# Kernel tuning notes

Hardware: AMD Instinct MI355X
Metric: run time of the kernel (lower is better)

## Reference

```python
import jax, jax.numpy as jnp
import numpy as np

WINDOW_SIZES = (128, 256, 512)
EMBED_DIM = 512
B, T = 128, 65536


def _branch_tokens(signal, W, b, w):
    # Conv1d(in=1, out=E, kernel=w, stride=w, padding=0) == non-overlapping
    # patch projection: (B, S, w) @ (w, E) with S = T // w.
    Bsz, Tlen = signal.shape
    S = Tlen // w
    patches = signal[:, : S * w].reshape(Bsz, S, w)
    return jnp.einsum('bsw,ew->bse', patches, W) + b  # (B, S, E)


def setup_inputs() -> dict:
    key = jax.random.key(0)
    ks = jax.random.split(key, 9)
    signal = jax.random.normal(ks[0], (B, T), dtype=jnp.float32)
    signal_mask = jax.random.randint(ks[1], (B, T), 0, 2).astype(bool)
    branch_idx = jax.random.randint(ks[2], (B,), 0, len(WINDOW_SIZES), dtype=jnp.int32)
    params = {}
    for i, w in enumerate(WINDOW_SIZES):
        params[f'W{i}'] = jax.random.normal(ks[3 + 2 * i], (EMBED_DIM, w), dtype=jnp.float32) * 0.02
        params[f'b{i}'] = jax.random.normal(ks[4 + 2 * i], (EMBED_DIM,), dtype=jnp.float32) * 0.02
    return {'signal': signal, 'signal_mask': signal_mask, 'branch_idx': branch_idx, **params}


def reference(signal, signal_mask, branch_idx, W0, b0, W1, b1, W2, b2):
    Bsz, Tlen = signal.shape
    Ws = (W0, W1, W2)
    bs = (b0, b1, b2)
    branch_S = [Tlen // w for w in WINDOW_SIZES]
    S_max = max(branch_S)
    # Compute every branch for every sample (faithful to the original module).
    padded = []
    for w, Wi, bi, Si in zip(WINDOW_SIZES, Ws, bs, branch_S):
        t = _branch_tokens(signal, Wi, bi, w)  # (B, Si, E)
        padded.append(jnp.pad(t, ((0, 0), (0, S_max - Si), (0, 0))))
    stacked = jnp.stack(padded)  # (n_branches, B, S_max, E)
    gathered = stacked[branch_idx, jnp.arange(Bsz)]  # (B, S_max, E)

    lengths = signal_mask.astype(jnp.int32).sum(axis=1)  # (B,)
    w_arr = jnp.asarray(WINDOW_SIZES, dtype=jnp.int32)
    S_arr = jnp.asarray(branch_S, dtype=jnp.int32)
    n_valid = jnp.minimum(lengths // w_arr[branch_idx],
                          jnp.minimum(S_arr[branch_idx], S_max))  # (B,)
    padding_mask = jnp.arange(S_max, dtype=jnp.int32)[None, :] < n_valid[:, None]  # (B, S_max)
    tokens = jnp.where(padding_mask[..., None], gathered, jnp.zeros((), signal.dtype))
    return tokens, padding_mask
```

## Files before the change

### kernel.cpp

```cpp
#include <hip/hip_runtime.h>
#include <hip/hip_bf16.h>

#define BATCH 128
#define TLEN  65536
#define EDIM  512
#define SMAX  512

typedef __attribute__((ext_vector_type(8))) short   bf16x8;
typedef __attribute__((ext_vector_type(4))) float   floatx4;
typedef __attribute__((ext_vector_type(8))) ushort  ushort8;

#define LDS_STRIDE 40
#define BUFSZ (128 * LDS_STRIDE)

__device__ __forceinline__ ushort f2bf(float f) {
  __hip_bfloat16 h = __float2bfloat16(f);
  return *reinterpret_cast<ushort*>(&h);
}

__device__ __forceinline__ void cvt16(ushort* dst, float4 a, float4 b,
                                      float4 c, float4 d) {
  ushort8 p0, p1;
  p0[0]=f2bf(a.x); p0[1]=f2bf(a.y); p0[2]=f2bf(a.z); p0[3]=f2bf(a.w);
  p0[4]=f2bf(b.x); p0[5]=f2bf(b.y); p0[6]=f2bf(b.z); p0[7]=f2bf(b.w);
  p1[0]=f2bf(c.x); p1[1]=f2bf(c.y); p1[2]=f2bf(c.z); p1[3]=f2bf(c.w);
  p1[4]=f2bf(d.x); p1[5]=f2bf(d.y); p1[6]=f2bf(d.z); p1[7]=f2bf(d.w);
  *(ushort8*)dst = p0; *(ushort8*)(dst + 8) = p1;
}

__global__ __launch_bounds__(256) void mask_partial_kernel(
    const int* __restrict__ mask, int* __restrict__ part) {
  const int b = blockIdx.x, c = blockIdx.y, t = threadIdx.x;
  const int4* row = (const int4*)(mask + (size_t)b * TLEN + (size_t)c * 8192);
  int s = 0;
  #pragma unroll
  for (int i = 0; i < 8; ++i) {
    int4 v = row[t + i * 256];
    s += (v.x != 0) + (v.y != 0) + (v.z != 0) + (v.w != 0);
  }
  #pragma unroll
  for (int off = 32; off > 0; off >>= 1) s += __shfl_down(s, off);
  __shared__ int partial[4];
  if ((t & 63) == 0) partial[t >> 6] = s;
  __syncthreads();
  if (t == 0)
    part[b * 8 + c] = partial[0] + partial[1] + partial[2] + partial[3];
}

__global__ __launch_bounds__(256) void mask_final_kernel(
    const int* __restrict__ part, const int* __restrict__ branch_idx,
    int* __restrict__ n_valid, float* __restrict__ out_mask) {
  const int b = blockIdx.x, t = threadIdx.x;
  __shared__ int nv_sh;
  if (t == 0) {
    int len = 0;
    #pragma unroll
    for (int i = 0; i < 8; ++i) len += part[b * 8 + i];
    int w = 128 << branch_idx[b];
    int nv = len / w;
    n_valid[b] = nv;
    nv_sh = nv;
  }
  __syncthreads();
  const int nv = nv_sh;
  out_mask[(size_t)b * SMAX + t]       = (t < nv)       ? 1.0f : 0.0f;
  out_mask[(size_t)b * SMAX + 256 + t] = (256 + t < nv) ? 1.0f : 0.0f;
}

template <int W>
__device__ __forceinline__ void gemm_body(
    const float* __restrict__ sigb, const float* __restrict__ Wp,
    const float* __restrict__ bp, float* __restrict__ outb,
    int nv, int s0, int e0, int t, ushort* Ab, ushort* Bb) {
  constexpr int ITERS = W / 32;
  const int wave   = t >> 6;
  const int lane   = t & 63;
  const int lane16 = lane & 15;
  const int quad   = lane >> 4;
  const int ws_ = (wave >> 1) * 64;
  const int we_ = (wave & 1) * 64;
  const int r = t >> 1, h = t & 1;

  const float* asrc = sigb + (size_t)(s0 + r) * W + h * 16;
  const float* bsrc = Wp + (size_t)(e0 + r) * W + h * 16;
  ushort* adst = Ab + r * LDS_STRIDE + h * 16;
  ushort* bdst = Bb + r * LDS_STRIDE + h * 16;

  float4 av0, av1, av2, av3, bv0, bv1, bv2, bv3;
  {
    const float4* a4 = (const float4*)asrc;
    const float4* b4 = (const float4*)bsrc;
    av0 = a4[0]; av1 = a4[1]; av2 = a4[2]; av3 = a4[3];
    bv0 = b4[0]; bv1 = b4[1]; bv2 = b4[2]; bv3 = b4[3];
  }
  cvt16(adst, av0, av1, av2, av3);
  cvt16(bdst, bv0, bv1, bv2, bv3);
  __syncthreads();

  floatx4 acc[4][4];
  #pragma unroll
  for (int i = 0; i < 4; ++i)
    #pragma unroll
    for (int j = 0; j < 4; ++j) acc[i][j] = (floatx4)(0.f);

  #pragma unroll
  for (int k = 0; k < ITERS; ++k) {
    const ushort* curA = Ab + (k & 1) * BUFSZ;
    const ushort* curB = Bb + (k & 1) * BUFSZ;
    if (k + 1 < ITERS) {
      const float4* a4 = (const float4*)(asrc + (k + 1) * 32);
      const float4* b4 = (const float4*)(bsrc + (k + 1) * 32);
      av0 = a4[0]; av1 = a4[1]; av2 = a4[2]; av3 = a4[3];
      bv0 = b4[0]; bv1 = b4[1]; bv2 = b4[2]; bv3 = b4[3];
    }
    bf16x8 af[4], bfr[4];
    #pragma unroll
    for (int i = 0; i < 4; ++i)
      af[i] = *(const bf16x8*)&curA[(ws_ + i * 16 + lane16) * LDS_STRIDE + quad * 8];
    #pragma unroll
    for (int j = 0; j < 4; ++j)
      bfr[j] = *(const bf16x8*)&curB[(we_ + j * 16 + lane16) * LDS_STRIDE + quad * 8];
    #pragma unroll
    for (int i = 0; i < 4; ++i)
      #pragma unroll
      for (int j = 0; j < 4; ++j)
        acc[i][j] = __builtin_amdgcn_mfma_f32_16x16x32_bf16(af[i], bfr[j], acc[i][j], 0, 0, 0);
    if (k + 1 < ITERS) {
      ushort* nA = Ab + ((k + 1) & 1) * BUFSZ + r * LDS_STRIDE + h * 16;
      ushort* nB = Bb + ((k + 1) & 1) * BUFSZ + r * LDS_STRIDE + h * 16;
      cvt16(nA, av0, av1, av2, av3);
      cvt16(nB, bv0, bv1, bv2, bv3);
      __syncthreads();
    }
  }

  float bval[4];
  #pragma unroll
  for (int j = 0; j < 4; ++j) bval[j] = bp[e0 + we_ + j * 16 + lane16];
  #pragma unroll
  for (int i = 0; i < 4; ++i) {
    #pragma unroll
    for (int rr = 0; rr < 4; ++rr) {
      const int s_row = s0 + ws_ + i * 16 + quad * 4 + rr;
      const bool valid = s_row < nv;
      float* op = outb + (size_t)s_row * EDIM + e0 + we_ + lane16;
      #pragma unroll
      for (int j = 0; j < 4; ++j)
        op[j * 16] = valid ? (acc[i][j][rr] + bval[j]) : 0.f;
    }
  }
}

__global__ __launch_bounds__(256) void gemm_kernel(
    const float* __restrict__ signal, const int* __restrict__ branch_idx,
    const int* __restrict__ n_valid_arr,
    const float* __restrict__ W0, const float* __restrict__ bias0,
    const float* __restrict__ W1, const float* __restrict__ bias1,
    const float* __restrict__ W2, const float* __restrict__ bias2,
    float* __restrict__ out) {
  const int et = blockIdx.x;
  const int st = blockIdx.y;
  const int b  = blockIdx.z;
  const int t  = threadIdx.x;
  const int s0 = st * 128;
  const int e0 = et * 128;
  const int bi = branch_idx[b];
  const int S_b = 512 >> bi;
  float* outb = out + (size_t)b * SMAX * EDIM;

  if (s0 >= S_b) {
    const float4 z = make_float4(0.f, 0.f, 0.f, 0.f);
    #pragma unroll
    for (int i = 0; i < 16; ++i) {
      int idx = t + i * 256;
      int r = idx >> 5, c = idx & 31;
      *(float4*)(outb + (size_t)(s0 + r) * EDIM + e0 + c * 4) = z;
    }
    return;
  }

  __shared__ __align__(16) ushort Ab[2 * BUFSZ];
  __shared__ __align__(16) ushort Bb[2 * BUFSZ];
  const int nv = n_valid_arr[b];
  const float* sigb = signal + (size_t)b * TLEN;

  switch (bi) {
    case 0:
      gemm_body<128>(sigb, W0, bias0, outb, nv, s0, e0, t, Ab, Bb);
      break;
    case 1:
      gemm_body<256>(sigb, W1, bias1, outb, nv, s0, e0, t, Ab, Bb);
      break;
    default:
      gemm_body<512>(sigb, W2, bias2, outb, nv, s0, e0, t, Ab, Bb);
      break;
  }
}

extern "C" void kernel_launch(void* const* d_in, const int* in_sizes, int n_in,
                              void* d_out, int out_size, void* d_ws, size_t ws_size,
                              hipStream_t stream) {
  const float* signal = (const float*)d_in[0];
  const int*   mask   = (const int*)d_in[1];
  const int*   bidx   = (const int*)d_in[2];
  const float* W0 = (const float*)d_in[3];
  const float* b0 = (const float*)d_in[4];
  const float* W1 = (const float*)d_in[5];
  const float* b1 = (const float*)d_in[6];
  const float* W2 = (const float*)d_in[7];
  const float* b2 = (const float*)d_in[8];

  float* out_tokens = (float*)d_out;
  float* out_mask   = (float*)d_out + (size_t)BATCH * SMAX * EDIM;
  int*   n_valid    = (int*)d_ws;
  int*   part       = (int*)d_ws + 128;

  mask_partial_kernel<<<dim3(BATCH, 8), dim3(256), 0, stream>>>(mask, part);
  mask_final_kernel<<<dim3(BATCH), dim3(256), 0, stream>>>(part, bidx, n_valid, out_mask);
  gemm_kernel<<<dim3(4, 4, BATCH), dim3(256), 0, stream>>>(
      signal, bidx, n_valid, W0, b0, W1, b1, W2, b2, out_tokens);
}
```

Measured before the change: 262.3 us.

## Pre-convert inputs to bf16 and stream tiles via global_load_lds with swizzle

Adds a separate pass that converts the whole signal and all weight matrices to bf16 in workspace. The GEMM then loads tiles directly into LDS using global_load_lds with an XOR-swizzled layout, removing per-tile register conversion. This costs an extra full read of the fp32 signal (32 MB) plus a 16 MB write, and the GEMM then reads the bf16 copy back. The old fp32 path remains as a fallback when the workspace is too small.

```diff
diff --git a/kernel.cpp b/kernel.cpp
--- a/kernel.cpp
+++ b/kernel.cpp
@@ -9,9 +9,6 @@
 typedef __attribute__((ext_vector_type(8))) short   bf16x8;
 typedef __attribute__((ext_vector_type(4))) float   floatx4;
 typedef __attribute__((ext_vector_type(8))) ushort  ushort8;
-
-#define LDS_STRIDE 40
-#define BUFSZ (128 * LDS_STRIDE)
 
 __device__ __forceinline__ ushort f2bf(float f) {
   __hip_bfloat16 h = __float2bfloat16(f);
@@ -28,6 +25,12 @@
   *(ushort8*)dst = p0; *(ushort8*)(dst + 8) = p1;
 }
 
+__device__ __forceinline__ void gl_lds16(const ushort* g, ushort* l) {
+  __builtin_amdgcn_global_load_lds(
+      (const __attribute__((address_space(1))) void*)g,
+      (__attribute__((address_space(3))) void*)l, 16, 0, 0);
+}
+
 __global__ __launch_bounds__(256) void mask_partial_kernel(
     const int* __restrict__ mask, int* __restrict__ part) {
   const int b = blockIdx.x, c = blockIdx.y, t = threadIdx.x;
@@ -67,71 +70,84 @@
   out_mask[(size_t)b * SMAX + 256 + t] = (256 + t < nv) ? 1.0f : 0.0f;
 }
 
+#define SIGN  (BATCH * TLEN)
+#define W0N   (EDIM * 128)
+#define W1N   (EDIM * 256)
+#define W2N   (EDIM * 512)
+#define CVT_TOTAL (SIGN + W0N + W1N + W2N)
+
+__global__ __launch_bounds__(256) void cvt_kernel(
+    const float* __restrict__ sig, const float* __restrict__ W0,
+    const float* __restrict__ W1, const float* __restrict__ W2,
+    ushort* __restrict__ dst) {
+  const size_t i = ((size_t)blockIdx.x * 256 + threadIdx.x) * 16;
+  const float* src;
+  if (i < SIGN)                  src = sig + i;
+  else if (i < SIGN + W0N)       src = W0 + (i - SIGN);
+  else if (i < SIGN + W0N + W1N) src = W1 + (i - SIGN - W0N);
+  else                           src = W2 + (i - SIGN - W0N - W1N);
+  const float4* s4 = (const float4*)src;
+  cvt16(dst + i, s4[0], s4[1], s4[2], s4[3]);
+}
+
 template <int W>
-__device__ __forceinline__ void gemm_body(
-    const float* __restrict__ sigb, const float* __restrict__ Wp,
+__device__ __forceinline__ void gemm_mfma_body(
+    const ushort* __restrict__ sigb, const ushort* __restrict__ Wp,
     const float* __restrict__ bp, float* __restrict__ outb,
-    int nv, int s0, int e0, int t, ushort* Ab, ushort* Bb) {
+    int nv, int s0, int e0, int t, ushort* Abuf, ushort* Bbuf) {
   constexpr int ITERS = W / 32;
-  const int wave   = t >> 6;
-  const int lane   = t & 63;
-  const int lane16 = lane & 15;
-  const int quad   = lane >> 4;
-  const int ws_ = (wave >> 1) * 64;
-  const int we_ = (wave & 1) * 64;
-  const int r = t >> 1, h = t & 1;
-
-  const float* asrc = sigb + (size_t)(s0 + r) * W + h * 16;
-  const float* bsrc = Wp + (size_t)(e0 + r) * W + h * 16;
-  ushort* adst = Ab + r * LDS_STRIDE + h * 16;
-  ushort* bdst = Bb + r * LDS_STRIDE + h * 16;
-
-  float4 av0, av1, av2, av3, bv0, bv1, bv2, bv3;
+  const int wave = t >> 6, lane = t & 63;
+  const int lane16 = lane & 15, quad = lane >> 4;
+  const int ws_ = (wave >> 1) * 64, we_ = (wave & 1) * 64;
+
+  const int c0 = t,        r0 = c0 >> 2, kc0 = (c0 & 3) ^ (r0 & 3);
+  const int c1 = t + 256,  r1 = c1 >> 2, kc1 = (c1 & 3) ^ (r1 & 3);
+  const ushort* ag0 = sigb + (size_t)(s0 + r0) * W + kc0 * 8;
+  const ushort* ag1 = sigb + (size_t)(s0 + r1) * W + kc1 * 8;
+  const ushort* bg0 = Wp + (size_t)(e0 + r0) * W + kc0 * 8;
+  const ushort* bg1 = Wp + (size_t)(e0 + r1) * W + kc1 * 8;
+  ushort* al0 = Abuf + wave * 512;
+  ushort* al1 = Abuf + 2048 + wave * 512;
+  ushort* bl0 = Bbuf + wave * 512;
+  ushort* bl1 = Bbuf + 2048 + wave * 512;
+
+  floatx4 acc[4][4];
+  #pragma unroll
+  for (int i = 0; i < 4; ++i)
+    #pragma unroll
+    for (int j = 0; j < 4; ++j) acc[i][j] = (floatx4)(0.f);
+
   {
-    const float4* a4 = (const float4*)asrc;
-    const float4* b4 = (const float4*)bsrc;
-    av0 = a4[0]; av1 = a4[1]; av2 = a4[2]; av3 = a4[3];
-    bv0 = b4[0]; bv1 = b4[1]; bv2 = b4[2]; bv3 = b4[3];
-  }
-  cvt16(adst, av0, av1, av2, av3);
-  cvt16(bdst, bv0, bv1, bv2, bv3);
+    gl_lds16(ag0, al0); gl_lds16(ag1, al1);
+    gl_lds16(bg0, bl0); gl_lds16(bg1, bl1);
+  }
   __syncthreads();
 
-  floatx4 acc[4][4];
-  #pragma unroll
-  for (int i = 0; i < 4; ++i)
-    #pragma unroll
-    for (int j = 0; j < 4; ++j) acc[i][j] = (floatx4)(0.f);
+  const int slotq = (quad ^ (lane16 & 3)) * 8;
 
   #pragma unroll
   for (int k = 0; k < ITERS; ++k) {
-    const ushort* curA = Ab + (k & 1) * BUFSZ;
-    const ushort* curB = Bb + (k & 1) * BUFSZ;
     if (k + 1 < ITERS) {
-      const float4* a4 = (const float4*)(asrc + (k + 1) * 32);
-      const float4* b4 = (const float4*)(bsrc + (k + 1) * 32);
-      av0 = a4[0]; av1 = a4[1]; av2 = a4[2]; av3 = a4[3];
-      bv0 = b4[0]; bv1 = b4[1]; bv2 = b4[2]; bv3 = b4[3];
-    }
+      const size_t ko = (size_t)(k + 1) * 32;
+      const int p = ((k + 1) & 1) * 4096;
+      gl_lds16(ag0 + ko, al0 + p); gl_lds16(ag1 + ko, al1 + p);
+      gl_lds16(bg0 + ko, bl0 + p); gl_lds16(bg1 + ko, bl1 + p);
+    }
+    const ushort* A = Abuf + (k & 1) * 4096;
+    const ushort* B = Bbuf + (k & 1) * 4096;
     bf16x8 af[4], bfr[4];
     #pragma unroll
     for (int i = 0; i < 4; ++i)
-      af[i] = *(const bf16x8*)&curA[(ws_ + i * 16 + lane16) * LDS_STRIDE + quad * 8];
+      af[i] = *(const bf16x8*)&A[(ws_ + i * 16 + lane16) * 32 + slotq];
     #pragma unroll
     for (int j = 0; j < 4; ++j)
-      bfr[j] = *(const bf16x8*)&curB[(we_ + j * 16 + lane16) * LDS_STRIDE + quad * 8];
+      bfr[j] = *(const bf16x8*)&B[(we_ + j * 16 + lane16) * 32 + slotq];
     #pragma unroll
     for (int i = 0; i < 4; ++i)
       #pragma unroll
       for (int j = 0; j < 4; ++j)
         acc[i][j] = __builtin_amdgcn_mfma_f32_16x16x32_bf16(af[i], bfr[j], acc[i][j], 0, 0, 0);
-    if (k + 1 < ITERS) {
-      ushort* nA = Ab + ((k + 1) & 1) * BUFSZ + r * LDS_STRIDE + h * 16;
-      ushort* nB = Bb + ((k + 1) & 1) * BUFSZ + r * LDS_STRIDE + h * 16;
-      cvt16(nA, av0, av1, av2, av3);
-      cvt16(nB, bv0, bv1, bv2, bv3);
-      __syncthreads();
-    }
+    __syncthreads();
   }
 
   float bval[4];
@@ -151,23 +167,128 @@
   }
 }
 
-__global__ __launch_bounds__(256) void gemm_kernel(
+__global__ __launch_bounds__(256) void gemm_bf_kernel(
+    const ushort* __restrict__ sigbf, const int* __restrict__ branch_idx,
+    const int* __restrict__ n_valid_arr,
+    const ushort* __restrict__ W0b, const float* __restrict__ bias0,
+    const ushort* __restrict__ W1b, const float* __restrict__ bias1,
+    const ushort* __restrict__ W2b, const float* __restrict__ bias2,
+    float* __restrict__ out) {
+  const int et = blockIdx.x, st = blockIdx.y, b = blockIdx.z;
+  const int t = threadIdx.x;
+  const int s0 = st * 128, e0 = et * 128;
+  const int bi = branch_idx[b];
+  const int S_b = 512 >> bi;
+  float* outb = out + (size_t)b * SMAX * EDIM;
+
+  if (s0 >= S_b) {
+    const float4 z = make_float4(0.f, 0.f, 0.f, 0.f);
+    #pragma unroll
+    for (int i = 0; i < 16; ++i) {
+      int idx = t + i * 256;
+      int r = idx >> 5, c = idx & 31;
+      *(float4*)(outb + (size_t)(s0 + r) * EDIM + e0 + c * 4) = z;
+    }
+    return;
+  }
+
+  __shared__ __align__(16) ushort Abuf[2 * 4096];
+  __shared__ __align__(16) ushort Bbuf[2 * 4096];
+  const int nv = n_valid_arr[b];
+  const ushort* sigb = sigbf + (size_t)b * TLEN;
+  switch (bi) {
+    case 0:  gemm_mfma_body<128>(sigb, W0b, bias0, outb, nv, s0, e0, t, Abuf, Bbuf); break;
+    case 1:  gemm_mfma_body<256>(sigb, W1b, bias1, outb, nv, s0, e0, t, Abuf, Bbuf); break;
+    default: gemm_mfma_body<512>(sigb, W2b, bias2, outb, nv, s0, e0, t, Abuf, Bbuf); break;
+  }
+}
+
+#define LDS_STRIDE 40
+#define BUFSZ (128 * LDS_STRIDE)
+
+template <int W>
+__device__ __forceinline__ void gemm_fb_body(
+    const float* __restrict__ sigb, const float* __restrict__ Wp,
+    const float* __restrict__ bp, float* __restrict__ outb,
+    int nv, int s0, int e0, int t, ushort* Ab, ushort* Bb) {
+  constexpr int ITERS = W / 32;
+  const int wave = t >> 6, lane = t & 63;
+  const int lane16 = lane & 15, quad = lane >> 4;
+  const int ws_ = (wave >> 1) * 64, we_ = (wave & 1) * 64;
+  const int r = t >> 1, h = t & 1;
+  const float* asrc = sigb + (size_t)(s0 + r) * W + h * 16;
+  const float* bsrc = Wp + (size_t)(e0 + r) * W + h * 16;
+  {
+    const float4* a4 = (const float4*)asrc;
+    const float4* b4 = (const float4*)bsrc;
+    cvt16(Ab + r * LDS_STRIDE + h * 16, a4[0], a4[1], a4[2], a4[3]);
+    cvt16(Bb + r * LDS_STRIDE + h * 16, b4[0], b4[1], b4[2], b4[3]);
+  }
+  __syncthreads();
+  floatx4 acc[4][4];
+  #pragma unroll
+  for (int i = 0; i < 4; ++i)
+    #pragma unroll
+    for (int j = 0; j < 4; ++j) acc[i][j] = (floatx4)(0.f);
+  #pragma unroll
+  for (int k = 0; k < ITERS; ++k) {
+    const ushort* curA = Ab + (k & 1) * BUFSZ;
+    const ushort* curB = Bb + (k & 1) * BUFSZ;
+    float4 av0, av1, av2, av3, bv0, bv1, bv2, bv3;
+    if (k + 1 < ITERS) {
+      const float4* a4 = (const float4*)(asrc + (k + 1) * 32);
+      const float4* b4 = (const float4*)(bsrc + (k + 1) * 32);
+      av0 = a4[0]; av1 = a4[1]; av2 = a4[2]; av3 = a4[3];
+      bv0 = b4[0]; bv1 = b4[1]; bv2 = b4[2]; bv3 = b4[3];
+    }
+    bf16x8 af[4], bfr[4];
+    #pragma unroll
+    for (int i = 0; i < 4; ++i)
+      af[i] = *(const bf16x8*)&curA[(ws_ + i * 16 + lane16) * LDS_STRIDE + quad * 8];
+    #pragma unroll
+    for (int j = 0; j < 4; ++j)
+      bfr[j] = *(const bf16x8*)&curB[(we_ + j * 16 + lane16) * LDS_STRIDE + quad * 8];
+    #pragma unroll
+    for (int i = 0; i < 4; ++i)
+      #pragma unroll
+      for (int j = 0; j < 4; ++j)
+        acc[i][j] = __builtin_amdgcn_mfma_f32_16x16x32_bf16(af[i], bfr[j], acc[i][j], 0, 0, 0);
+    if (k + 1 < ITERS) {
+      cvt16(Ab + ((k + 1) & 1) * BUFSZ + r * LDS_STRIDE + h * 16, av0, av1, av2, av3);
+      cvt16(Bb + ((k + 1) & 1) * BUFSZ + r * LDS_STRIDE + h * 16, bv0, bv1, bv2, bv3);
+      __syncthreads();
+    }
+  }
+  float bval[4];
+  #pragma unroll
+  for (int j = 0; j < 4; ++j) bval[j] = bp[e0 + we_ + j * 16 + lane16];
+  #pragma unroll
+  for (int i = 0; i < 4; ++i) {
+    #pragma unroll
+    for (int rr = 0; rr < 4; ++rr) {
+      const int s_row = s0 + ws_ + i * 16 + quad * 4 + rr;
+      const bool valid = s_row < nv;
+      float* op = outb + (size_t)s_row * EDIM + e0 + we_ + lane16;
+      #pragma unroll
+      for (int j = 0; j < 4; ++j)
+        op[j * 16] = valid ? (acc[i][j][rr] + bval[j]) : 0.f;
+    }
+  }
+}
+
+__global__ __launch_bounds__(256) void gemm_fb_kernel(
     const float* __restrict__ signal, const int* __restrict__ branch_idx,
     const int* __restrict__ n_valid_arr,
     const float* __restrict__ W0, const float* __restrict__ bias0,
     const float* __restrict__ W1, const float* __restrict__ bias1,
     const float* __restrict__ W2, const float* __restrict__ bias2,
     float* __restrict__ out) {
-  const int et = blockIdx.x;
-  const int st = blockIdx.y;
-  const int b  = blockIdx.z;
-  const int t  = threadIdx.x;
-  const int s0 = st * 128;
-  const int e0 = et * 128;
+  const int et = blockIdx.x, st = blockIdx.y, b = blockIdx.z;
+  const int t = threadIdx.x;
+  const int s0 = st * 128, e0 = et * 128;
   const int bi = branch_idx[b];
   const int S_b = 512 >> bi;
   float* outb = out + (size_t)b * SMAX * EDIM;
-
   if (s0 >= S_b) {
     const float4 z = make_float4(0.f, 0.f, 0.f, 0.f);
     #pragma unroll
@@ -178,22 +299,14 @@
     }
     return;
   }
-
   __shared__ __align__(16) ushort Ab[2 * BUFSZ];
   __shared__ __align__(16) ushort Bb[2 * BUFSZ];
   const int nv = n_valid_arr[b];
   const float* sigb = signal + (size_t)b * TLEN;
-
   switch (bi) {
-    case 0:
-      gemm_body<128>(sigb, W0, bias0, outb, nv, s0, e0, t, Ab, Bb);
-      break;
-    case 1:
-      gemm_body<256>(sigb, W1, bias1, outb, nv, s0, e0, t, Ab, Bb);
-      break;
-    default:
-      gemm_body<512>(sigb, W2, bias2, outb, nv, s0, e0, t, Ab, Bb);
-      break;
+    case 0:  gemm_fb_body<128>(sigb, W0, bias0, outb, nv, s0, e0, t, Ab, Bb); break;
+    case 1:  gemm_fb_body<256>(sigb, W1, bias1, outb, nv, s0, e0, t, Ab, Bb); break;
+    default: gemm_fb_body<512>(sigb, W2, bias2, outb, nv, s0, e0, t, Ab, Bb); break;
   }
 }
 
@@ -217,6 +330,20 @@
 
   mask_partial_kernel<<<dim3(BATCH, 8), dim3(256), 0, stream>>>(mask, part);
   mask_final_kernel<<<dim3(BATCH), dim3(256), 0, stream>>>(part, bidx, n_valid, out_mask);
-  gemm_kernel<<<dim3(4, 4, BATCH), dim3(256), 0, stream>>>(
-      signal, bidx, n_valid, W0, b0, W1, b1, W2, b2, out_tokens);
-}
+
+  const size_t need = 8192 + (size_t)CVT_TOTAL * 2;
+  if (ws_size >= need) {
+    ushort* cvt_base = (ushort*)((char*)d_ws + 8192);
+    ushort* sig_bf = cvt_base;
+    ushort* w0_bf  = cvt_base + SIGN;
+    ushort* w1_bf  = w0_bf + W0N;
+    ushort* w2_bf  = w1_bf + W1N;
+    cvt_kernel<<<dim3(CVT_TOTAL / 4096), dim3(256), 0, stream>>>(
+        signal, W0, W1, W2, cvt_base);
+    gemm_bf_kernel<<<dim3(4, 4, BATCH), dim3(256), 0, stream>>>(
+        sig_bf, bidx, n_valid, w0_bf, b0, w1_bf, b1, w2_bf, b2, out_tokens);
+  } else {
+    gemm_fb_kernel<<<dim3(4, 4, BATCH), dim3(256), 0, stream>>>(
+        signal, bidx, n_valid, W0, b0, W1, b1, W2, b2, out_tokens);
+  }
+}
```

Result: faster. 223.0 us (-15.0%).
